# Kernel optimization log

Hardware: AMD Instinct MI355X
Metric: run time of the kernel (lower is better)

## Reference

```python
import jax, jax.numpy as jnp
import numpy as np

N_NODES = 50000
N_EDGES = 300000
D_IN = 256
D_HID = 256


def setup_inputs() -> dict:
    key = jax.random.key(0)
    ks = jax.random.split(key, 9)
    x = jax.random.normal(ks[0], (N_NODES, D_IN), dtype=jnp.float32)
    src = jax.random.randint(ks[1], (N_EDGES,), 0, N_NODES, dtype=jnp.int64)
    dst = jax.random.randint(ks[2], (N_EDGES,), 0, N_NODES, dtype=jnp.int64)
    # Kaiming-uniform-ish init like nn.Linear defaults
    def lin(k, fan_in, fan_out):
        bound = 1.0 / np.sqrt(fan_in)
        kw, kb = jax.random.split(k)
        W = jax.random.uniform(kw, (fan_out, fan_in), minval=-bound, maxval=bound, dtype=jnp.float32)
        b = jax.random.uniform(kb, (fan_out,), minval=-bound, maxval=bound, dtype=jnp.float32)
        return W, b
    W1, b1 = lin(ks[3], 2 * D_IN, D_HID)
    W2, b2 = lin(ks[4], D_HID, D_HID)
    W3, b3 = lin(ks[5], D_HID, 1)
    return {"x": x, "src": src, "dst": dst,
            "W1": W1, "b1": b1, "W2": W2, "b2": b2, "W3": W3, "b3": b3}


def reference(x, src, dst, W1, b1, W2, b2, W3, b3):
    # gather src/dst node features per edge and concat -> [E, 2*D_IN]
    h = jnp.concatenate([x[src], x[dst]], axis=1)
    h = jax.nn.relu(h @ W1.T + b1)          # [E, D_HID]
    h = jax.nn.relu(h @ W2.T + b2)          # dropout is identity in eval mode
    score = h @ W3.T + b3                   # [E, 1]
    return score
```

## Files before the change

kernel.cpp:

```cpp
#include <hip/hip_runtime.h>

typedef short bfx8 __attribute__((ext_vector_type(8)));
typedef float fx4 __attribute__((ext_vector_type(4)));

#define D 256
#define E_TILE 64

__device__ __forceinline__ float b2f(short s) {
  union { unsigned u; float f; } v; v.u = ((unsigned)(unsigned short)s) << 16; return v.f;
}
__device__ __forceinline__ short f2b(float f) {
  union { float f; unsigned u; } v; v.f = f;
  unsigned u = v.u;
  u += 0x7fffu + ((u >> 16) & 1u);
  return (short)(u >> 16);
}
__device__ __forceinline__ float relu(float f) { return f > 0.f ? f : 0.f; }
__device__ __forceinline__ float asf(unsigned u) { union { unsigned u; float f; } v; v.u = u; return v.f; }
__device__ __forceinline__ unsigned asu(float f) { union { float f; unsigned u; } v; v.f = f; return v.u; }

__global__ void k_prep(const float* __restrict__ W1, const float* __restrict__ W2,
                       unsigned short* __restrict__ B1, unsigned short* __restrict__ W2b) {
  int t = blockIdx.x * 256 + threadIdx.x;
  if (t < 512 * 256) {
    int n = t >> 8, k = t & 255;
    float v = (n < 256) ? W1[n * 512 + k] : W1[(n - 256) * 512 + 256 + k];
    B1[t] = (unsigned short)f2b(v);
  } else if (t < 512 * 256 + 256 * 256) {
    int i = t - 512 * 256;
    W2b[i] = (unsigned short)f2b(W2[i]);
  }
}

__launch_bounds__(256, 2)
__global__ void k_node(const float* __restrict__ x, const unsigned short* __restrict__ B1,
                       const float* __restrict__ b1,
                       unsigned short* __restrict__ PQ, int n_nodes) {
  __shared__ __align__(16) short smA[64 * 40];
  __shared__ __align__(16) short smW[512 * 40];
  short* smT = smW;
  const int tid = threadIdx.x;
  const int wave = tid >> 6, lane = tid & 63;
  const int lr = lane & 15, lg = lane >> 4;
  const int m0 = blockIdx.x * 64;

  fx4 acc[4][8] = {};

#pragma unroll 1
  for (int ks = 0; ks < 8; ++ks) {
    const int k0 = ks * 32;
    {
      int r = tid >> 2, c = (tid & 3) * 8;
      int m = m0 + r;
      bfx8 o;
      if (m < n_nodes) {
        const float* p = x + (size_t)m * 256 + k0 + c;
        float4 v0 = *(const float4*)(p);
        float4 v1 = *(const float4*)(p + 4);
        o[0] = f2b(v0.x); o[1] = f2b(v0.y); o[2] = f2b(v0.z); o[3] = f2b(v0.w);
        o[4] = f2b(v1.x); o[5] = f2b(v1.y); o[6] = f2b(v1.z); o[7] = f2b(v1.w);
      } else {
        o = (bfx8){0,0,0,0,0,0,0,0};
      }
      *(bfx8*)&smA[r * 40 + c] = o;
    }
#pragma unroll
    for (int it = 0; it < 8; ++it) {
      int idx = it * 256 + tid;
      int n = idx >> 2, c = (idx & 3) * 8;
      bfx8 v = *(const bfx8*)(B1 + n * 256 + k0 + c);
      *(bfx8*)&smW[n * 40 + c] = v;
    }
    __syncthreads();
    bfx8 af[4];
#pragma unroll
    for (int mt = 0; mt < 4; ++mt)
      af[mt] = *(const bfx8*)&smA[(mt * 16 + lr) * 40 + lg * 8];
#pragma unroll
    for (int nt = 0; nt < 8; ++nt) {
      int n = wave * 128 + nt * 16 + lr;
      bfx8 bf = *(const bfx8*)&smW[n * 40 + lg * 8];
#pragma unroll
      for (int mt = 0; mt < 4; ++mt)
        acc[mt][nt] = __builtin_amdgcn_mfma_f32_16x16x32_bf16(af[mt], bf, acc[mt][nt], 0, 0, 0);
    }
    __syncthreads();
  }

  float bias[8];
#pragma unroll
  for (int nt = 0; nt < 8; ++nt) {
    int n = wave * 128 + nt * 16 + lr;
    bias[nt] = (n >= 256) ? b1[n - 256] : 0.f;
  }

#pragma unroll
  for (int h = 0; h < 2; ++h) {
#pragma unroll
    for (int mt2 = 0; mt2 < 2; ++mt2) {
      const int mt = 2 * h + mt2;
#pragma unroll
      for (int nt = 0; nt < 8; ++nt)
#pragma unroll
        for (int i = 0; i < 4; ++i) {
          int mrow = mt2 * 16 + lg * 4 + i;
          int n = wave * 128 + nt * 16 + lr;
          smT[mrow * 520 + n] = f2b(acc[mt][nt][i] + bias[nt]);
        }
    }
    __syncthreads();
    int r = tid >> 3, cbase = (tid & 7) * 8;
    int m = m0 + h * 32 + r;
    if (m < n_nodes) {
#pragma unroll
      for (int j = 0; j < 8; ++j) {
        int c = cbase + j * 64;
        *(bfx8*)(PQ + (size_t)m * 512 + c) = *(const bfx8*)&smT[r * 520 + c];
      }
    }
    __syncthreads();
  }
}

__launch_bounds__(256, 2)
__global__ void k_edge(const unsigned short* __restrict__ PQ,
                       const int* __restrict__ src, const int* __restrict__ dst,
                       const unsigned short* __restrict__ W2b,
                       const float* __restrict__ b2, const float* __restrict__ W3,
                       const float* __restrict__ b3, float* __restrict__ out,
                       int E, int ntiles) {
  __shared__ __align__(16) short smH[64 * 264];
  __shared__ float smS[4][64];
  const int tid = threadIdx.x;
  const int wave = tid >> 6, lane = tid & 63;
  const int lr = lane & 15, lg = lane >> 4;

  bfx8 bw[4][8];
  float b2v[4], w3v[4];
#pragma unroll
  for (int nt = 0; nt < 4; ++nt) {
    int n = wave * 64 + nt * 16 + lr;
    b2v[nt] = b2[n];
    w3v[nt] = W3[n];
#pragma unroll
    for (int ks = 0; ks < 8; ++ks)
      bw[nt][ks] = *(const bfx8*)(W2b + n * 256 + ks * 32 + lg * 8);
  }
  const float b3v = b3[0];

  for (int tile = blockIdx.x; tile < ntiles; tile += gridDim.x) {
    const int base = tile * E_TILE;
    {
      int r = tid >> 2;
      int e = base + r;
      if (e < E) {
        int s = src[e], d = dst[e];
        const unsigned* ps = (const unsigned*)(PQ + (size_t)s * 512);
        const unsigned* pd = (const unsigned*)(PQ + (size_t)d * 512 + 256);
#pragma unroll
        for (int it = 0; it < 8; ++it) {
          int c = (tid & 3) * 8 + it * 32;
          uint4 pv = *(const uint4*)(ps + (c >> 1));
          uint4 qv = *(const uint4*)(pd + (c >> 1));
          unsigned o[4];
          const unsigned* pw = (const unsigned*)&pv;
          const unsigned* qw = (const unsigned*)&qv;
#pragma unroll
          for (int w = 0; w < 4; ++w) {
            unsigned up = pw[w], uq = qw[w];
            float slo = relu(asf(up << 16) + asf(uq << 16));
            float shi = relu(asf(up & 0xffff0000u) + asf(uq & 0xffff0000u));
            o[w] = __builtin_amdgcn_perm(asu(shi) + 0x8000u, asu(slo) + 0x8000u,
                                         0x07060302u);
          }
          *(uint4*)&smH[r * 264 + c] = make_uint4(o[0], o[1], o[2], o[3]);
        }
      } else {
#pragma unroll
        for (int it = 0; it < 8; ++it) {
          int c = (tid & 3) * 8 + it * 32;
          *(uint4*)&smH[r * 264 + c] = make_uint4(0, 0, 0, 0);
        }
      }
    }
    __syncthreads();

    fx4 acc[4][4] = {};
#pragma unroll
    for (int ks = 0; ks < 8; ++ks) {
      bfx8 af[4];
#pragma unroll
      for (int mt = 0; mt < 4; ++mt)
        af[mt] = *(const bfx8*)&smH[(mt * 16 + lr) * 264 + ks * 32 + lg * 8];
#pragma unroll
      for (int nt = 0; nt < 4; ++nt)
#pragma unroll
        for (int mt = 0; mt < 4; ++mt)
          acc[mt][nt] = __builtin_amdgcn_mfma_f32_16x16x32_bf16(af[mt], bw[nt][ks], acc[mt][nt], 0, 0, 0);
    }

#pragma unroll
    for (int mt = 0; mt < 4; ++mt)
#pragma unroll
      for (int i = 0; i < 4; ++i) {
        float p = 0.f;
#pragma unroll
        for (int nt = 0; nt < 4; ++nt)
          p += relu(acc[mt][nt][i] + b2v[nt]) * w3v[nt];
        p += __shfl_xor(p, 1);
        p += __shfl_xor(p, 2);
        p += __shfl_xor(p, 4);
        p += __shfl_xor(p, 8);
        if (lr == 0) smS[wave][mt * 16 + lg * 4 + i] = p;
      }
    __syncthreads();
    if (tid < 64) {
      int e = base + tid;
      if (e < E) out[e] = smS[0][tid] + smS[1][tid] + smS[2][tid] + smS[3][tid] + b3v;
    }
    __syncthreads();
  }
}

__global__ void k_fallback(const float* __restrict__ x, const int* __restrict__ src,
                           const int* __restrict__ dst, const float* __restrict__ W1,
                           const float* __restrict__ b1, const float* __restrict__ W2,
                           const float* __restrict__ b2, const float* __restrict__ W3,
                           const float* __restrict__ b3, float* __restrict__ out, int E) {
  __shared__ float smF[4][512];
  __shared__ float smG[4][256];
  int wave = threadIdx.x >> 6, lane = threadIdx.x & 63;
  int e = blockIdx.x * 4 + wave;
  bool valid = e < E;
  int ec = valid ? e : 0;
  int s = src[ec], d = dst[ec];
  for (int j = 0; j < 8; ++j) {
    int k = lane * 8 + j;
    smF[wave][k] = (k < 256) ? x[(size_t)s * 256 + k] : x[(size_t)d * 256 + k - 256];
  }
  __syncthreads();
  for (int t = 0; t < 4; ++t) {
    int n = lane + t * 64;
    float a = b1[n];
    for (int k = 0; k < 512; ++k) a += smF[wave][k] * W1[n * 512 + k];
    smG[wave][n] = relu(a);
  }
  __syncthreads();
  float p = 0.f;
  for (int t = 0; t < 4; ++t) {
    int n = lane + t * 64;
    float a = b2[n];
    for (int k = 0; k < 256; ++k) a += smG[wave][k] * W2[n * 256 + k];
    p += relu(a) * W3[n];
  }
  for (int m = 1; m < 64; m <<= 1) p += __shfl_xor(p, m);
  if (lane == 0 && valid) out[e] = p + b3[0];
}

extern "C" void kernel_launch(void* const* d_in, const int* in_sizes, int n_in,
                              void* d_out, int out_size, void* d_ws, size_t ws_size,
                              hipStream_t stream) {
  const float* x  = (const float*)d_in[0];
  const int*   src = (const int*)d_in[1];
  const int*   dst = (const int*)d_in[2];
  const float* W1 = (const float*)d_in[3];
  const float* b1 = (const float*)d_in[4];
  const float* W2 = (const float*)d_in[5];
  const float* b2 = (const float*)d_in[6];
  const float* W3 = (const float*)d_in[7];
  const float* b3 = (const float*)d_in[8];
  float* out = (float*)d_out;

  const int E = in_sizes[1];
  const int n_nodes = in_sizes[0] / 256;

  const size_t offB1 = 0;
  const size_t offW2 = (size_t)512 * 256 * 2;
  const size_t offPQ = offW2 + (size_t)256 * 256 * 2;
  const size_t need = offPQ + (size_t)n_nodes * 512 * 2;

  if (ws_size >= need) {
    unsigned short* B1  = (unsigned short*)((char*)d_ws + offB1);
    unsigned short* W2b = (unsigned short*)((char*)d_ws + offW2);
    unsigned short* PQ  = (unsigned short*)((char*)d_ws + offPQ);
    k_prep<<<768, 256, 0, stream>>>(W1, W2, B1, W2b);
    k_node<<<(n_nodes + 63) / 64, 256, 0, stream>>>(x, B1, b1, PQ, n_nodes);
    const int ntiles = (E + E_TILE - 1) / E_TILE;
    int grid = ntiles < 1024 ? ntiles : 1024;
    k_edge<<<grid, 256, 0, stream>>>(PQ, src, dst, W2b, b2, W3, b3, out, E, ntiles);
  } else {
    k_fallback<<<(E + 3) / 4, 256, 0, stream>>>(x, src, dst, W1, b1, W2, b2, W3, b3, out, E);
  }
}
```

Before: 236.1 us.

## Double block size to 8 waves in node and edge kernels, prefetch edge indices

Both the node GEMM and the edge MLP kernels move from 4 to 8 waves per block. Each wave now owns half as many output columns, so per-thread accumulators and register-resident W2 fragments shrink and more waves can be resident. The edge kernel also loads the src/dst indices for its next tile before the current tile's MMA phase, hiding index-load latency. The edge grid is halved to 512 blocks. The trade-off is more LDS traffic per MFMA (A fragments are re-read by twice as many waves) and a wider final reduction across 8 partial sums.

```diff
diff --git a/kernel.cpp b/kernel.cpp
--- a/kernel.cpp
+++ b/kernel.cpp
@@ -1,14 +1,11 @@
 #include <hip/hip_runtime.h>
 
 typedef short bfx8 __attribute__((ext_vector_type(8)));
+typedef short bfx4 __attribute__((ext_vector_type(4)));
 typedef float fx4 __attribute__((ext_vector_type(4)));
 
-#define D 256
 #define E_TILE 64
 
-__device__ __forceinline__ float b2f(short s) {
-  union { unsigned u; float f; } v; v.u = ((unsigned)(unsigned short)s) << 16; return v.f;
-}
 __device__ __forceinline__ short f2b(float f) {
   union { float f; unsigned u; } v; v.f = f;
   unsigned u = v.u;
@@ -32,7 +29,7 @@
   }
 }
 
-__launch_bounds__(256, 2)
+__launch_bounds__(512, 4)
 __global__ void k_node(const float* __restrict__ x, const unsigned short* __restrict__ B1,
                        const float* __restrict__ b1,
                        unsigned short* __restrict__ PQ, int n_nodes) {
@@ -44,32 +41,28 @@
   const int lr = lane & 15, lg = lane >> 4;
   const int m0 = blockIdx.x * 64;
 
-  fx4 acc[4][8] = {};
+  fx4 acc[4][4] = {};
 
 #pragma unroll 1
   for (int ks = 0; ks < 8; ++ks) {
     const int k0 = ks * 32;
     {
-      int r = tid >> 2, c = (tid & 3) * 8;
+      int r = tid >> 3, c = (tid & 7) * 4;
       int m = m0 + r;
-      bfx8 o;
+      bfx4 o;
       if (m < n_nodes) {
-        const float* p = x + (size_t)m * 256 + k0 + c;
-        float4 v0 = *(const float4*)(p);
-        float4 v1 = *(const float4*)(p + 4);
-        o[0] = f2b(v0.x); o[1] = f2b(v0.y); o[2] = f2b(v0.z); o[3] = f2b(v0.w);
-        o[4] = f2b(v1.x); o[5] = f2b(v1.y); o[6] = f2b(v1.z); o[7] = f2b(v1.w);
+        float4 v = *(const float4*)(x + (size_t)m * 256 + k0 + c);
+        o[0] = f2b(v.x); o[1] = f2b(v.y); o[2] = f2b(v.z); o[3] = f2b(v.w);
       } else {
-        o = (bfx8){0,0,0,0,0,0,0,0};
-      }
-      *(bfx8*)&smA[r * 40 + c] = o;
-    }
-#pragma unroll
-    for (int it = 0; it < 8; ++it) {
-      int idx = it * 256 + tid;
+        o = (bfx4){0, 0, 0, 0};
+      }
+      *(bfx4*)&smA[r * 40 + c] = o;
+    }
+#pragma unroll
+    for (int it = 0; it < 4; ++it) {
+      int idx = it * 512 + tid;
       int n = idx >> 2, c = (idx & 3) * 8;
-      bfx8 v = *(const bfx8*)(B1 + n * 256 + k0 + c);
-      *(bfx8*)&smW[n * 40 + c] = v;
+      *(bfx8*)&smW[n * 40 + c] = *(const bfx8*)(B1 + n * 256 + k0 + c);
     }
     __syncthreads();
     bfx8 af[4];
@@ -77,9 +70,8 @@
     for (int mt = 0; mt < 4; ++mt)
       af[mt] = *(const bfx8*)&smA[(mt * 16 + lr) * 40 + lg * 8];
 #pragma unroll
-    for (int nt = 0; nt < 8; ++nt) {
-      int n = wave * 128 + nt * 16 + lr;
-      bfx8 bf = *(const bfx8*)&smW[n * 40 + lg * 8];
+    for (int nt = 0; nt < 4; ++nt) {
+      bfx8 bf = *(const bfx8*)&smW[(wave * 64 + nt * 16 + lr) * 40 + lg * 8];
 #pragma unroll
       for (int mt = 0; mt < 4; ++mt)
         acc[mt][nt] = __builtin_amdgcn_mfma_f32_16x16x32_bf16(af[mt], bf, acc[mt][nt], 0, 0, 0);
@@ -87,10 +79,10 @@
     __syncthreads();
   }
 
-  float bias[8];
-#pragma unroll
-  for (int nt = 0; nt < 8; ++nt) {
-    int n = wave * 128 + nt * 16 + lr;
+  float bias[4];
+#pragma unroll
+  for (int nt = 0; nt < 4; ++nt) {
+    int n = wave * 64 + nt * 16 + lr;
     bias[nt] = (n >= 256) ? b1[n - 256] : 0.f;
   }
 
@@ -100,21 +92,21 @@
     for (int mt2 = 0; mt2 < 2; ++mt2) {
       const int mt = 2 * h + mt2;
 #pragma unroll
-      for (int nt = 0; nt < 8; ++nt)
+      for (int nt = 0; nt < 4; ++nt)
 #pragma unroll
         for (int i = 0; i < 4; ++i) {
           int mrow = mt2 * 16 + lg * 4 + i;
-          int n = wave * 128 + nt * 16 + lr;
+          int n = wave * 64 + nt * 16 + lr;
           smT[mrow * 520 + n] = f2b(acc[mt][nt][i] + bias[nt]);
         }
     }
     __syncthreads();
-    int r = tid >> 3, cbase = (tid & 7) * 8;
+    int r = tid >> 4, cbase = (tid & 15) * 8;
     int m = m0 + h * 32 + r;
     if (m < n_nodes) {
 #pragma unroll
-      for (int j = 0; j < 8; ++j) {
-        int c = cbase + j * 64;
+      for (int j = 0; j < 4; ++j) {
+        int c = cbase + j * 128;
         *(bfx8*)(PQ + (size_t)m * 512 + c) = *(const bfx8*)&smT[r * 520 + c];
       }
     }
@@ -122,7 +114,7 @@
   }
 }
 
-__launch_bounds__(256, 2)
+__launch_bounds__(512, 4)
 __global__ void k_edge(const unsigned short* __restrict__ PQ,
                        const int* __restrict__ src, const int* __restrict__ dst,
                        const unsigned short* __restrict__ W2b,
@@ -130,16 +122,16 @@
                        const float* __restrict__ b3, float* __restrict__ out,
                        int E, int ntiles) {
   __shared__ __align__(16) short smH[64 * 264];
-  __shared__ float smS[4][64];
+  __shared__ float smS[8][64];
   const int tid = threadIdx.x;
   const int wave = tid >> 6, lane = tid & 63;
   const int lr = lane & 15, lg = lane >> 4;
 
-  bfx8 bw[4][8];
-  float b2v[4], w3v[4];
-#pragma unroll
-  for (int nt = 0; nt < 4; ++nt) {
-    int n = wave * 64 + nt * 16 + lr;
+  bfx8 bw[2][8];
+  float b2v[2], w3v[2];
+#pragma unroll
+  for (int nt = 0; nt < 2; ++nt) {
+    int n = wave * 32 + nt * 16 + lr;
     b2v[nt] = b2[n];
     w3v[nt] = W3[n];
 #pragma unroll
@@ -148,44 +140,49 @@
   }
   const float b3v = b3[0];
 
+  const int r = tid >> 3;
+  const int stride = gridDim.x * E_TILE;
+
+  int e0 = blockIdx.x * E_TILE + r;
+  int s_cur = 0, d_cur = 0;
+  if (e0 < E) { s_cur = src[e0]; d_cur = dst[e0]; }
+
   for (int tile = blockIdx.x; tile < ntiles; tile += gridDim.x) {
     const int base = tile * E_TILE;
-    {
-      int r = tid >> 2;
-      int e = base + r;
-      if (e < E) {
-        int s = src[e], d = dst[e];
-        const unsigned* ps = (const unsigned*)(PQ + (size_t)s * 512);
-        const unsigned* pd = (const unsigned*)(PQ + (size_t)d * 512 + 256);
-#pragma unroll
-        for (int it = 0; it < 8; ++it) {
-          int c = (tid & 3) * 8 + it * 32;
-          uint4 pv = *(const uint4*)(ps + (c >> 1));
-          uint4 qv = *(const uint4*)(pd + (c >> 1));
-          unsigned o[4];
-          const unsigned* pw = (const unsigned*)&pv;
-          const unsigned* qw = (const unsigned*)&qv;
-#pragma unroll
-          for (int w = 0; w < 4; ++w) {
-            unsigned up = pw[w], uq = qw[w];
-            float slo = relu(asf(up << 16) + asf(uq << 16));
-            float shi = relu(asf(up & 0xffff0000u) + asf(uq & 0xffff0000u));
-            o[w] = __builtin_amdgcn_perm(asu(shi) + 0x8000u, asu(slo) + 0x8000u,
-                                         0x07060302u);
-          }
-          *(uint4*)&smH[r * 264 + c] = make_uint4(o[0], o[1], o[2], o[3]);
+    const int e = base + r;
+    if (e < E) {
+      const unsigned* ps = (const unsigned*)(PQ + (size_t)s_cur * 512);
+      const unsigned* pd = (const unsigned*)(PQ + (size_t)d_cur * 512 + 256);
+#pragma unroll
+      for (int it = 0; it < 4; ++it) {
+        int c = (tid & 7) * 8 + it * 64;
+        uint4 pv = *(const uint4*)(ps + (c >> 1));
+        uint4 qv = *(const uint4*)(pd + (c >> 1));
+        unsigned o[4];
+        const unsigned* pw = (const unsigned*)&pv;
+        const unsigned* qw = (const unsigned*)&qv;
+#pragma unroll
+        for (int w = 0; w < 4; ++w) {
+          unsigned up = pw[w], uq = qw[w];
+          float slo = relu(asf(up << 16) + asf(uq << 16));
+          float shi = relu(asf(up & 0xffff0000u) + asf(uq & 0xffff0000u));
+          o[w] = __builtin_amdgcn_perm(asu(shi) + 0x8000u, asu(slo) + 0x8000u,
+                                       0x07060302u);
         }
-      } else {
-#pragma unroll
-        for (int it = 0; it < 8; ++it) {
-          int c = (tid & 3) * 8 + it * 32;
-          *(uint4*)&smH[r * 264 + c] = make_uint4(0, 0, 0, 0);
-        }
-      }
-    }
-    __syncthreads();
-
-    fx4 acc[4][4] = {};
+        *(uint4*)&smH[r * 264 + c] = make_uint4(o[0], o[1], o[2], o[3]);
+      }
+    } else {
+#pragma unroll
+      for (int it = 0; it < 4; ++it) {
+        int c = (tid & 7) * 8 + it * 64;
+        *(uint4*)&smH[r * 264 + c] = make_uint4(0, 0, 0, 0);
+      }
+    }
+    int e_next = e + stride;
+    if (e_next < E) { s_cur = src[e_next]; d_cur = dst[e_next]; }
+    __syncthreads();
+
+    fx4 acc[4][2] = {};
 #pragma unroll
     for (int ks = 0; ks < 8; ++ks) {
       bfx8 af[4];
@@ -193,7 +190,7 @@
       for (int mt = 0; mt < 4; ++mt)
         af[mt] = *(const bfx8*)&smH[(mt * 16 + lr) * 264 + ks * 32 + lg * 8];
 #pragma unroll
-      for (int nt = 0; nt < 4; ++nt)
+      for (int nt = 0; nt < 2; ++nt)
 #pragma unroll
         for (int mt = 0; mt < 4; ++mt)
           acc[mt][nt] = __builtin_amdgcn_mfma_f32_16x16x32_bf16(af[mt], bw[nt][ks], acc[mt][nt], 0, 0, 0);
@@ -205,7 +202,7 @@
       for (int i = 0; i < 4; ++i) {
         float p = 0.f;
 #pragma unroll
-        for (int nt = 0; nt < 4; ++nt)
+        for (int nt = 0; nt < 2; ++nt)
           p += relu(acc[mt][nt][i] + b2v[nt]) * w3v[nt];
         p += __shfl_xor(p, 1);
         p += __shfl_xor(p, 2);
@@ -215,8 +212,10 @@
       }
     __syncthreads();
     if (tid < 64) {
-      int e = base + tid;
-      if (e < E) out[e] = smS[0][tid] + smS[1][tid] + smS[2][tid] + smS[3][tid] + b3v;
+      int eo = base + tid;
+      if (eo < E)
+        out[eo] = smS[0][tid] + smS[1][tid] + smS[2][tid] + smS[3][tid] +
+                  smS[4][tid] + smS[5][tid] + smS[6][tid] + smS[7][tid] + b3v;
     }
     __syncthreads();
   }
@@ -284,10 +283,10 @@
     unsigned short* W2b = (unsigned short*)((char*)d_ws + offW2);
     unsigned short* PQ  = (unsigned short*)((char*)d_ws + offPQ);
     k_prep<<<768, 256, 0, stream>>>(W1, W2, B1, W2b);
-    k_node<<<(n_nodes + 63) / 64, 256, 0, stream>>>(x, B1, b1, PQ, n_nodes);
+    k_node<<<(n_nodes + 63) / 64, 512, 0, stream>>>(x, B1, b1, PQ, n_nodes);
     const int ntiles = (E + E_TILE - 1) / E_TILE;
-    int grid = ntiles < 1024 ? ntiles : 1024;
-    k_edge<<<grid, 256, 0, stream>>>(PQ, src, dst, W2b, b2, W3, b3, out, E, ntiles);
+    int grid = ntiles < 512 ? ntiles : 512;
+    k_edge<<<grid, 512, 0, stream>>>(PQ, src, dst, W2b, b2, W3, b3, out, E, ntiles);
   } else {
     k_fallback<<<(E + 3) / 4, 256, 0, stream>>>(x, src, dst, W1, b1, W2, b2, W3, b3, out, E);
   }
```

Result: no change. 235.6 us (-0.2%).
